# Kernel tuning notes

Measured on AMD Instinct MI355X. Metric: run time of the kernel, lower is better.

The kernel has to match this reference:

```python
import jax, jax.numpy as jnp
import numpy as np
from jax import lax

EPS = 1e-5
N_WIRES, N_LAYERS = 4, 3
DIM = 2 ** N_WIRES  # 16

# Static CNOT permutations for control w, target w+1 (state @ CNOT => new[k] = old[k ^ (((k>>c)&1)<<t)])
_idx = np.arange(DIM)
CNOT_PERMS = [jnp.asarray(_idx ^ (((_idx >> w) & 1) << (w + 1))) for w in range(N_WIRES - 1)]


def conv3x3(x, w):
    # x: [B,1,H,W], w: [1,1,3,3], padding=1, no bias
    return lax.conv_general_dilated(x, w, (1, 1), 'SAME',
                                    dimension_numbers=('NCHW', 'OIHW', 'NCHW'))


def batchnorm_train(x, gamma, beta):
    # training-mode BN: batch statistics over (B,H,W), biased variance
    mean = jnp.mean(x, axis=(0, 2, 3), keepdims=True)
    var = jnp.var(x, axis=(0, 2, 3), keepdims=True)
    xn = (x - mean) * lax.rsqrt(var + EPS)
    return xn * gamma.reshape(1, -1, 1, 1) + beta.reshape(1, -1, 1, 1)


def residual_block(x, w1, g1, b1, w2, g2, b2):
    out = jax.nn.relu(batchnorm_train(conv3x3(x, w1), g1, b1))
    out = batchnorm_train(conv3x3(out, w2), g2, b2)
    return jax.nn.relu(out + x)


def quantum_feat4(theta):
    # Faithful to QuantumKernel: real state, each RZ scales by cos(theta/2)
    # (rz[0,0]==rz[1,1]==cos(theta/2)), CNOT is a bit-indexed permutation.
    # State is independent of the patch values (patch is never used).
    s = jnp.zeros(DIM, dtype=theta.dtype).at[0].set(1.0)
    for l in range(N_LAYERS):
        s = s * jnp.prod(jnp.cos(theta[l] / 2.0))  # 8 RZ scalings for this layer
        for w in range(N_WIRES - 1):
            s = s[CNOT_PERMS[w]]
    probs = s ** 2
    return probs[:4]


def setup_inputs() -> dict:
    key = jax.random.key(0)
    ks = jax.random.split(key, 12)
    B = 16384
    d = dict(
        x=jax.random.normal(ks[0], (B, 1, 28, 28), dtype=jnp.float32),
        theta=jax.random.normal(ks[1], (N_LAYERS, N_WIRES, 2), dtype=jnp.float32),
        r1_w1=jax.random.normal(ks[2], (1, 1, 3, 3), dtype=jnp.float32) * 0.3,
        r1_g1=jnp.ones((1,), jnp.float32), r1_b1=jnp.zeros((1,), jnp.float32),
        r1_w2=jax.random.normal(ks[3], (1, 1, 3, 3), dtype=jnp.float32) * 0.3,
        r1_g2=jnp.ones((1,), jnp.float32), r1_b2=jnp.zeros((1,), jnp.float32),
        r2_w1=jax.random.normal(ks[4], (1, 1, 3, 3), dtype=jnp.float32) * 0.3,
        r2_g1=jnp.ones((1,), jnp.float32), r2_b1=jnp.zeros((1,), jnp.float32),
        r2_w2=jax.random.normal(ks[5], (1, 1, 3, 3), dtype=jnp.float32) * 0.3,
        r2_g2=jnp.ones((1,), jnp.float32), r2_b2=jnp.zeros((1,), jnp.float32),
        fc_w=jax.random.normal(ks[6], (10, 784), dtype=jnp.float32) * 0.03,
        fc_b=jnp.zeros((10,), jnp.float32),
        alpha=jnp.asarray(0.5, dtype=jnp.float32),
    )
    return d


def reference(x, theta, r1_w1, r1_g1, r1_b1, r1_w2, r1_g2, r1_b2,
              r2_w1, r2_g1, r2_b1, r2_w2, r2_g2, r2_b2, fc_w, fc_b, alpha):
    B = x.shape[0]
    cls_feat = residual_block(x, r1_w1, r1_g1, r1_b1, r1_w2, r1_g2, r1_b2)
    cls_feat = residual_block(cls_feat, r2_w1, r2_g1, r2_b1, r2_w2, r2_g2, r2_b2)
    cls_flat = cls_feat.reshape(B, -1)  # [B, 784]

    # Quantum filter: kernel output ignores patch values, identical for all
    # 196 patches and all batch elements; cat along dim=1 -> tile the 4-vector.
    p4 = quantum_feat4(theta)                           # [4]
    q_feat = jnp.broadcast_to(jnp.tile(p4, 14 * 14), (B, 784))

    fused = alpha * cls_flat + (1.0 - alpha) * q_feat
    logits = fused @ fc_w.T + fc_b
    return jax.nn.log_softmax(logits, axis=-1)
```

## Files before the change

### kernel.cpp

```cpp
#include <hip/hip_runtime.h>
#include <hip/hip_fp16.h>
#include <math.h>

#define BATCH   16384
#define IMGPIX  784
#define NTOT    (BATCH * IMGPIX)
#define NSLOT   64
#define SLOTSTR 8
#define STAGE_DBL (NSLOT * SLOTSTR)
#define TROW 224
#define TGRP 6272

struct __align__(8) h4 { __half2 lo, hi; };
__device__ __forceinline__ h4 f4_to_h4(float4 v) {
    h4 r; r.lo = __floats2half2_rn(v.x, v.y); r.hi = __floats2half2_rn(v.z, v.w); return r;
}
__device__ __forceinline__ float4 h4_to_f4(h4 p) {
    float2 a = __half22float2(p.lo), b = __half22float2(p.hi);
    return make_float4(a.x, a.y, b.x, b.y);
}

__device__ __forceinline__ void wave_stats_atomic(double lsum, double lsq, double* slot) {
    #pragma unroll
    for (int off = 32; off >= 1; off >>= 1) {
        lsum += __shfl_down(lsum, off, 64);
        lsq  += __shfl_down(lsq,  off, 64);
    }
    if ((threadIdx.x & 63) == 0) {
        atomicAdd(&slot[0], lsum);
        atomicAdd(&slot[1], lsq);
    }
}

__device__ __forceinline__ float2 stats_ab(const double* __restrict__ stats_in,
                                           float gamma, float beta) {
    int lane = threadIdx.x & 63;
    double s = stats_in[lane * SLOTSTR];
    double q = stats_in[lane * SLOTSTR + 1];
    #pragma unroll
    for (int off = 32; off >= 1; off >>= 1) {
        s += __shfl_down(s, off, 64);
        q += __shfl_down(q, off, 64);
    }
    s = __shfl(s, 0, 64);
    q = __shfl(q, 0, 64);
    const double INV_N = 1.0 / (double)NTOT;
    double mean = s * INV_N;
    double var  = q * INV_N - mean * mean;
    float rstd = 1.0f / sqrtf((float)var + 1e-5f);
    float a  = gamma * rstd;
    float bb = beta - (float)mean * a;
    return make_float2(a, bb);
}

__device__ __forceinline__ float4 hrow(float wl, float wc, float wr,
                                       float L, float4 v, float R) {
    float4 h;
    h.x = fmaf(wl, L,   fmaf(wc, v.x, wr * v.y));
    h.y = fmaf(wl, v.x, fmaf(wc, v.y, wr * v.z));
    h.z = fmaf(wl, v.y, fmaf(wc, v.z, wr * v.w));
    h.w = fmaf(wl, v.z, fmaf(wc, v.w, wr * R));
    return h;
}

__device__ __forceinline__ void emit_row(__half* dst, int r, float4 o, float mf,
                                         double& lsum, double& lsq, bool act) {
    if (act) *(h4*)(dst + r * TROW) = f4_to_h4(o);
    float s4 = (o.x + o.y) + (o.z + o.w);
    float q4 = fmaf(o.x, o.x, fmaf(o.y, o.y, fmaf(o.z, o.z, o.w * o.w)));
    lsum += (double)(mf * s4);
    lsq  += (double)(mf * q4);
}

#define LANE_SETUP()                                                          \
    const int t = threadIdx.x;                                                \
    const int lane = t & 63;                                                  \
    const int widx = t >> 6;                                                  \
    const int c4   = lane & 7;                                                \
    const bool act = (c4 < 7);                                                \
    const float mf = act ? 1.f : 0.f;                                         \
    const int c4c  = c4 < 7 ? c4 : 6;          \
    const int g    = blockIdx.x & 511;                 \
    const int s    = blockIdx.x >> 9;                         \
    const int r0   = s * 7;                                                   \
    const int rtop = (r0 > 0)  ? (r0 - 1) : 0;         \
    const int rbot = (r0 < 21) ? (r0 + 7) : 27;                               \
    const int i8   = lane >> 3;                                               \
    const int G    = g * 4 + widx;                 \
    const int img  = G * 8 + i8;                                              \
    const size_t xbase = (size_t)img * IMGPIX + c4c * 4;           \
    const size_t tbR   = (size_t)G * TGRP + c4c * 32 + i8 * 4;     \
    const size_t tbW   = (size_t)G * TGRP + c4  * 32 + i8 * 4;

#define CONV_STEP(k, v)                                                       \
    {                                                                         \
        float L = __shfl_up((v).w, 1, 64);  if (c4 == 0) L = 0.f;             \
        float R = __shfl_down((v).x, 1, 64); if (c4 == 6) R = 0.f;            \
        float4 h2 = hrow(w9[6], w9[7], w9[8], L, (v), R);                     \
        float4 h1 = hrow(w9[3], w9[4], w9[5], L, (v), R);                     \
        float4 h0 = hrow(w9[0], w9[1], w9[2], L, (v), R);                     \
        accA.x += h2.x; accA.y += h2.y; accA.z += h2.z; accA.w += h2.w;       \
        if ((k) >= 2) emit_row(dst, r0 + (k) - 2, accA, mf, lsum, lsq, act);  \
        accA.x = accB.x + h1.x; accA.y = accB.y + h1.y;                       \
        accA.z = accB.z + h1.z; accA.w = accB.w + h1.w;                       \
        accB = h0;                                                            \
    }

#define HALO_ZERO(k, v)                                                       \
    if ((k) == 0 && r0 == 0)  (v) = ZERO4;                                    \
    if ((k) == 8 && r0 == 21) (v) = ZERO4;

#define ZERO4 make_float4(0.f, 0.f, 0.f, 0.f)

__global__ __launch_bounds__(256, 8) void k_conv_plain(const float* __restrict__ in,
        const float* __restrict__ w, __half* __restrict__ out, double* __restrict__ stats_out)
{
    LANE_SETUP();
    float w9[9];
    #pragma unroll
    for (int i = 0; i < 9; i++) w9[i] = w[i];
    const float* src = in + xbase;
    __half* dst = out + tbW;

    float4 vb[9];
    vb[0] = *(const float4*)(src + rtop * 28);
    #pragma unroll
    for (int k = 1; k < 8; k++) vb[k] = *(const float4*)(src + (r0 - 1 + k) * 28);
    vb[8] = *(const float4*)(src + rbot * 28);
    __builtin_amdgcn_sched_barrier(0);

    float4 accA = ZERO4, accB = ZERO4;
    double lsum = 0.0, lsq = 0.0;
    #pragma unroll
    for (int k = 0; k < 9; k++) {
        float4 v = vb[k];
        HALO_ZERO(k, v);
        CONV_STEP(k, v);
    }
    wave_stats_atomic(lsum, lsq, &stats_out[((blockIdx.x * 4 + widx) & (NSLOT - 1)) * SLOTSTR]);
}

__global__ __launch_bounds__(256, 8) void k_conv_affine(const __half* __restrict__ in,
        const double* __restrict__ stats_in,
        const float* __restrict__ gamma, const float* __restrict__ beta,
        const float* __restrict__ w, __half* __restrict__ out, double* __restrict__ stats_out)
{
    LANE_SETUP();
    float2 ab = stats_ab(stats_in, gamma[0], beta[0]);
    float w9[9];
    #pragma unroll
    for (int i = 0; i < 9; i++) w9[i] = w[i];
    const __half* src = in + tbR;
    __half* dst = out + tbW;

    h4 vb[9];
    vb[0] = *(const h4*)(src + rtop * TROW);
    #pragma unroll
    for (int k = 1; k < 8; k++) vb[k] = *(const h4*)(src + (r0 - 1 + k) * TROW);
    vb[8] = *(const h4*)(src + rbot * TROW);
    __builtin_amdgcn_sched_barrier(0);

    float4 accA = ZERO4, accB = ZERO4;
    double lsum = 0.0, lsq = 0.0;
    #pragma unroll
    for (int k = 0; k < 9; k++) {
        float4 r4 = h4_to_f4(vb[k]);
        float4 v;
        v.x = fmaxf(fmaf(ab.x, r4.x, ab.y), 0.f);
        v.y = fmaxf(fmaf(ab.x, r4.y, ab.y), 0.f);
        v.z = fmaxf(fmaf(ab.x, r4.z, ab.y), 0.f);
        v.w = fmaxf(fmaf(ab.x, r4.w, ab.y), 0.f);
        HALO_ZERO(k, v);
        CONV_STEP(k, v);
    }
    wave_stats_atomic(lsum, lsq, &stats_out[((blockIdx.x * 4 + widx) & (NSLOT - 1)) * SLOTSTR]);
}

__global__ __launch_bounds__(256, 6) void k_conv_resid(const __half* __restrict__ y2,
        const float* __restrict__ x, const double* __restrict__ stats_in,
        const float* __restrict__ gamma, const float* __restrict__ beta,
        const float* __restrict__ w, __half* __restrict__ y3_out,
        __half* __restrict__ o1_out, double* __restrict__ stats_out)
{
    LANE_SETUP();
    float2 ab = stats_ab(stats_in, gamma[0], beta[0]);
    float w9[9];
    #pragma unroll
    for (int i = 0; i < 9; i++) w9[i] = w[i];
    const __half* srcy = y2 + tbR;
    const float*  srcx = x + xbase;
    __half* dst  = y3_out + tbW;
    __half* dsto = o1_out + tbW;

    h4 yb[9];
    float4 xb[9];
    yb[0] = *(const h4*)(srcy + rtop * TROW);
    xb[0] = *(const float4*)(srcx + rtop * 28);
    #pragma unroll
    for (int k = 1; k < 8; k++) {
        yb[k] = *(const h4*)(srcy + (r0 - 1 + k) * TROW);
        xb[k] = *(const float4*)(srcx + (r0 - 1 + k) * 28);
    }
    yb[8] = *(const h4*)(srcy + rbot * TROW);
    xb[8] = *(const float4*)(srcx + rbot * 28);
    __builtin_amdgcn_sched_barrier(0);

    float4 accA = ZERO4, accB = ZERO4;
    double lsum = 0.0, lsq = 0.0;
    #pragma unroll
    for (int k = 0; k < 9; k++) {
        float4 r4 = h4_to_f4(yb[k]);
        float4 x4 = xb[k];
        float4 v;
        v.x = fmaxf(fmaf(ab.x, r4.x, ab.y) + x4.x, 0.f);
        v.y = fmaxf(fmaf(ab.x, r4.y, ab.y) + x4.y, 0.f);
        v.z = fmaxf(fmaf(ab.x, r4.z, ab.y) + x4.z, 0.f);
        v.w = fmaxf(fmaf(ab.x, r4.w, ab.y) + x4.w, 0.f);
        HALO_ZERO(k, v);
        if (act && k >= 1 && k <= 7)
            *(h4*)(dsto + (r0 - 1 + k) * TROW) = f4_to_h4(v);
        CONV_STEP(k, v);
    }
    wave_stats_atomic(lsum, lsq, &stats_out[((blockIdx.x * 4 + widx) & (NSLOT - 1)) * SLOTSTR]);
}

__global__ __launch_bounds__(256) void k_head(const __half* __restrict__ y4,
        const __half* __restrict__ o1, const double* __restrict__ stats_in,
        const float* __restrict__ gamma, const float* __restrict__ beta,
        const float* __restrict__ fc_w, const float* __restrict__ qk,
        const float* __restrict__ alpha_p, float* __restrict__ out)
{
    __shared__ float fcK[7840];
    const int t = threadIdx.x;
    float2 ab = stats_ab(stats_in, gamma[0], beta[0]);
    for (int idx = t; idx < 7840; idx += 256) fcK[idx] = fc_w[idx];
    float alpha = alpha_p[0];
    float qkr[10];
    #pragma unroll
    for (int k = 0; k < 10; k++) qkr[k] = qk[k];
    __syncthreads();

    const int lane = t & 63;
    const int widx = t >> 6;
    const int c4   = lane & 7;
    const int i8   = lane >> 3;
    const int c4c  = c4 < 7 ? c4 : 6;
    const float mf = (c4 < 7) ? 1.f : 0.f;
    const int G    = blockIdx.x * 4 + widx;
    const size_t tb = (size_t)G * TGRP + c4c * 32 + i8 * 4;
    const __half* ya = y4 + tb;
    const __half* oa = o1 + tb;

    float acc[10];
    #pragma unroll
    for (int k = 0; k < 10; k++) acc[k] = 0.f;

    #pragma unroll 7
    for (int r = 0; r < 28; r++) {
        float4 yf = h4_to_f4(*(const h4*)(ya + r * TROW));
        float4 of = h4_to_f4(*(const h4*)(oa + r * TROW));
        float4 v;
        v.x = fmaxf(fmaf(ab.x, yf.x, ab.y) + of.x, 0.f);
        v.y = fmaxf(fmaf(ab.x, yf.y, ab.y) + of.y, 0.f);
        v.z = fmaxf(fmaf(ab.x, yf.z, ab.y) + of.z, 0.f);
        v.w = fmaxf(fmaf(ab.x, yf.w, ab.y) + of.w, 0.f);
        const float* fb = &fcK[r * 28 + c4c * 4];
        #pragma unroll
        for (int k = 0; k < 10; k++) {
            const float4 f = *(const float4*)(fb + k * 784);
            acc[k] = fmaf(v.x, f.x, fmaf(v.y, f.y, fmaf(v.z, f.z, fmaf(v.w, f.w, acc[k]))));
        }
    }
    #pragma unroll
    for (int k = 0; k < 10; k++) {
        acc[k] *= mf;
        acc[k] += __shfl_xor(acc[k], 1, 64);
        acc[k] += __shfl_xor(acc[k], 2, 64);
        acc[k] += __shfl_xor(acc[k], 4, 64);
    }
    float l[10];
    float m = -1e30f;
    #pragma unroll
    for (int k = 0; k < 10; k++) {
        l[k] = fmaf(alpha, acc[k], qkr[k]);
        m = fmaxf(m, l[k]);
    }
    float se = 0.f;
    #pragma unroll
    for (int k = 0; k < 10; k++) se += __expf(l[k] - m);
    float lse = m + __logf(se);
    if (c4 == 0) {
        int img = G * 8 + i8;
        #pragma unroll
        for (int k = 0; k < 10; k++) out[(size_t)img * 10 + k] = l[k] - lse;
    }
}

__global__ __launch_bounds__(256) void k_init(const float* __restrict__ theta,
        const float* __restrict__ fc_w, const float* __restrict__ fc_b,
        const float* __restrict__ alpha_p, float* __restrict__ qk, double* __restrict__ stats)
{
    const int t = threadIdx.x;
    for (int i = t; i < 4 * STAGE_DBL; i += 256) stats[i] = 0.0;
    if (t < 10) {
        float c = 1.f;
        #pragma unroll
        for (int i = 0; i < 24; i++) c *= cosf(theta[i] * 0.5f);
        float c2 = c * c;
        float s = 0.f;
        for (int j = 0; j < 784; j += 4) s += fc_w[t * 784 + j];
        qk[t] = (1.f - alpha_p[0]) * c2 * s + fc_b[t];
    }
}

extern "C" void kernel_launch(void* const* d_in, const int* in_sizes, int n_in,
                              void* d_out, int out_size, void* d_ws, size_t ws_size,
                              hipStream_t stream) {
    const float* x     = (const float*)d_in[0];
    const float* theta = (const float*)d_in[1];
    const float* r1_w1 = (const float*)d_in[2];
    const float* r1_g1 = (const float*)d_in[3];
    const float* r1_b1 = (const float*)d_in[4];
    const float* r1_w2 = (const float*)d_in[5];
    const float* r1_g2 = (const float*)d_in[6];
    const float* r1_b2 = (const float*)d_in[7];
    const float* r2_w1 = (const float*)d_in[8];
    const float* r2_g1 = (const float*)d_in[9];
    const float* r2_b1 = (const float*)d_in[10];
    const float* r2_w2 = (const float*)d_in[11];
    const float* r2_g2 = (const float*)d_in[12];
    const float* r2_b2 = (const float*)d_in[13];
    const float* fc_w  = (const float*)d_in[14];
    const float* fc_b  = (const float*)d_in[15];
    const float* alpha = (const float*)d_in[16];
    float* out = (float*)d_out;

    double* stats = (double*)d_ws;
    float*  qk    = (float*)((char*)d_ws + 16384);
    __half* bufA  = (__half*)((char*)d_ws + 32768);
    __half* bufB  = bufA + (size_t)NTOT;
    __half* bufD  = bufB + (size_t)NTOT;

    double* s_y1 = stats + 0 * STAGE_DBL;
    double* s_y2 = stats + 1 * STAGE_DBL;
    double* s_y3 = stats + 2 * STAGE_DBL;
    double* s_y4 = stats + 3 * STAGE_DBL;

    k_init<<<1, 256, 0, stream>>>(theta, fc_w, fc_b, alpha, qk, stats);
    k_conv_plain<<<2048, 256, 0, stream>>>(x, r1_w1, bufA, s_y1);
    k_conv_affine<<<2048, 256, 0, stream>>>(bufA, s_y1, r1_g1, r1_b1, r1_w2, bufB, s_y2);
    k_conv_resid<<<2048, 256, 0, stream>>>(bufB, x, s_y2, r1_g2, r1_b2, r2_w1, bufA, bufD, s_y3);
    k_conv_affine<<<2048, 256, 0, stream>>>(bufA, s_y3, r2_g1, r2_b1, r2_w2, bufB, s_y4);
    k_head<<<512, 256, 0, stream>>>(bufB, bufD, s_y4, r2_g2, r2_b2, fc_w, qk, alpha, out);
}
```

Baseline: 108.5 us.

## Cache fp16 copy of input in first conv for residual reuse

The first conv kernel now also writes a half-precision copy of the input image, and the residual conv kernel reads that copy instead of the fp32 input. This halves the bytes read for the residual operand at the cost of an extra fp16 write in the first pass, and allows raising the residual kernel's occupancy hint to 8. The init kernel's per-class fc_w strided sum is parallelised across 80 threads with shuffle reductions instead of a serial loop. The residual add now uses fp16-rounded inputs, which adds precision error.

```diff
diff --git a/kernel.cpp b/kernel.cpp
--- a/kernel.cpp
+++ b/kernel.cpp
@@ -113,14 +113,16 @@
 #define ZERO4 make_float4(0.f, 0.f, 0.f, 0.f)
 
 __global__ __launch_bounds__(256, 8) void k_conv_plain(const float* __restrict__ in,
-        const float* __restrict__ w, __half* __restrict__ out, double* __restrict__ stats_out)
+        const float* __restrict__ w, __half* __restrict__ out,
+        __half* __restrict__ x16_out, double* __restrict__ stats_out)
 {
     LANE_SETUP();
     float w9[9];
     #pragma unroll
     for (int i = 0; i < 9; i++) w9[i] = w[i];
     const float* src = in + xbase;
-    __half* dst = out + tbW;
+    __half* dst  = out + tbW;
+    __half* dstx = x16_out + tbW;
 
     float4 vb[9];
     vb[0] = *(const float4*)(src + rtop * 28);
@@ -134,6 +136,8 @@
     #pragma unroll
     for (int k = 0; k < 9; k++) {
         float4 v = vb[k];
+        if (act && k >= 1 && k <= 7)
+            *(h4*)(dstx + (r0 - 1 + k) * TROW) = f4_to_h4(vb[k]);
         HALO_ZERO(k, v);
         CONV_STEP(k, v);
     }
@@ -176,8 +180,8 @@
     wave_stats_atomic(lsum, lsq, &stats_out[((blockIdx.x * 4 + widx) & (NSLOT - 1)) * SLOTSTR]);
 }
 
-__global__ __launch_bounds__(256, 6) void k_conv_resid(const __half* __restrict__ y2,
-        const float* __restrict__ x, const double* __restrict__ stats_in,
+__global__ __launch_bounds__(256, 8) void k_conv_resid(const __half* __restrict__ y2,
+        const __half* __restrict__ x16, const double* __restrict__ stats_in,
         const float* __restrict__ gamma, const float* __restrict__ beta,
         const float* __restrict__ w, __half* __restrict__ y3_out,
         __half* __restrict__ o1_out, double* __restrict__ stats_out)
@@ -188,21 +192,20 @@
     #pragma unroll
     for (int i = 0; i < 9; i++) w9[i] = w[i];
     const __half* srcy = y2 + tbR;
-    const float*  srcx = x + xbase;
+    const __half* srcx = x16 + tbR;
     __half* dst  = y3_out + tbW;
     __half* dsto = o1_out + tbW;
 
-    h4 yb[9];
-    float4 xb[9];
+    h4 yb[9], xb[9];
     yb[0] = *(const h4*)(srcy + rtop * TROW);
-    xb[0] = *(const float4*)(srcx + rtop * 28);
+    xb[0] = *(const h4*)(srcx + rtop * TROW);
     #pragma unroll
     for (int k = 1; k < 8; k++) {
         yb[k] = *(const h4*)(srcy + (r0 - 1 + k) * TROW);
-        xb[k] = *(const float4*)(srcx + (r0 - 1 + k) * 28);
+        xb[k] = *(const h4*)(srcx + (r0 - 1 + k) * TROW);
     }
     yb[8] = *(const h4*)(srcy + rbot * TROW);
-    xb[8] = *(const float4*)(srcx + rbot * 28);
+    xb[8] = *(const h4*)(srcx + rbot * TROW);
     __builtin_amdgcn_sched_barrier(0);
 
     float4 accA = ZERO4, accB = ZERO4;
@@ -210,7 +213,7 @@
     #pragma unroll
     for (int k = 0; k < 9; k++) {
         float4 r4 = h4_to_f4(yb[k]);
-        float4 x4 = xb[k];
+        float4 x4 = h4_to_f4(xb[k]);
         float4 v;
         v.x = fmaxf(fmaf(ab.x, r4.x, ab.y) + x4.x, 0.f);
         v.y = fmaxf(fmaf(ab.x, r4.y, ab.y) + x4.y, 0.f);
@@ -302,14 +305,27 @@
 {
     const int t = threadIdx.x;
     for (int i = t; i < 4 * STAGE_DBL; i += 256) stats[i] = 0.0;
+    __shared__ float csum[10];
+    if (t < 80) {
+        int k = t >> 3, oct = t & 7;
+        float s = 0.f;
+        #pragma unroll
+        for (int i = 0; i < 25; i++) {
+            int p = oct + 8 * i;
+            if (p < 196) s += fc_w[k * 784 + p * 4];
+        }
+        s += __shfl_xor(s, 1, 64);
+        s += __shfl_xor(s, 2, 64);
+        s += __shfl_xor(s, 4, 64);
+        if (oct == 0) csum[k] = s;
+    }
+    __syncthreads();
     if (t < 10) {
         float c = 1.f;
         #pragma unroll
         for (int i = 0; i < 24; i++) c *= cosf(theta[i] * 0.5f);
         float c2 = c * c;
-        float s = 0.f;
-        for (int j = 0; j < 784; j += 4) s += fc_w[t * 784 + j];
-        qk[t] = (1.f - alpha_p[0]) * c2 * s + fc_b[t];
+        qk[t] = (1.f - alpha_p[0]) * c2 * csum[t] + fc_b[t];
     }
 }
 
@@ -340,6 +356,7 @@
     __half* bufA  = (__half*)((char*)d_ws + 32768);
     __half* bufB  = bufA + (size_t)NTOT;
     __half* bufD  = bufB + (size_t)NTOT;
+    __half* bufX  = bufD + (size_t)NTOT;
 
     double* s_y1 = stats + 0 * STAGE_DBL;
     double* s_y2 = stats + 1 * STAGE_DBL;
@@ -347,9 +364,9 @@
     double* s_y4 = stats + 3 * STAGE_DBL;
 
     k_init<<<1, 256, 0, stream>>>(theta, fc_w, fc_b, alpha, qk, stats);
-    k_conv_plain<<<2048, 256, 0, stream>>>(x, r1_w1, bufA, s_y1);
+    k_conv_plain<<<2048, 256, 0, stream>>>(x, r1_w1, bufA, bufX, s_y1);
     k_conv_affine<<<2048, 256, 0, stream>>>(bufA, s_y1, r1_g1, r1_b1, r1_w2, bufB, s_y2);
-    k_conv_resid<<<2048, 256, 0, stream>>>(bufB, x, s_y2, r1_g2, r1_b2, r2_w1, bufA, bufD, s_y3);
+    k_conv_resid<<<2048, 256, 0, stream>>>(bufB, bufX, s_y2, r1_g2, r1_b2, r2_w1, bufA, bufD, s_y3);
     k_conv_affine<<<2048, 256, 0, stream>>>(bufA, s_y3, r2_g1, r2_b1, r2_w2, bufB, s_y4);
     k_head<<<512, 256, 0, stream>>>(bufB, bufD, s_y4, r2_g2, r2_b2, fc_w, qk, alpha, out);
 }
```

Result: no change. 107.2 us (-1.2%).
